# Kernel tuning notes

Measured on AMD Instinct MI355X. Metric: run time of the kernel, lower is better.

Reference implementation:

```python
import jax, jax.numpy as jnp
import numpy as np

N, C, H, W = 16, 256, 64, 64
KC, VC, HEADS = 256, 256, 8

def setup_inputs() -> dict:
    key = jax.random.key(0)
    ks = jax.random.split(key, 9)
    s = 0.02
    return {
        "x": jax.random.normal(ks[0], (N, C, H, W), dtype=jnp.float32),
        "Wk": jax.random.normal(ks[1], (KC, C), dtype=jnp.float32) * s,
        "bk": jax.random.normal(ks[2], (KC,), dtype=jnp.float32) * s,
        "Wq": jax.random.normal(ks[3], (KC, C), dtype=jnp.float32) * s,
        "bq": jax.random.normal(ks[4], (KC,), dtype=jnp.float32) * s,
        "Wv": jax.random.normal(ks[5], (VC, C), dtype=jnp.float32) * s,
        "bv": jax.random.normal(ks[6], (VC,), dtype=jnp.float32) * s,
        "Wr": jax.random.normal(ks[7], (C, VC), dtype=jnp.float32) * s,
        "br": jax.random.normal(ks[8], (C,), dtype=jnp.float32) * s,
    }

def reference(x, Wk, bk, Wq, bq, Wv, bv, Wr, br):
    n, c, h, w = x.shape
    hw = h * w
    hk = KC // HEADS   # per-head key channels
    hv = VC // HEADS   # per-head value channels
    # 1x1 convs as channel matmuls
    keys = jnp.einsum('oi,nihw->nohw', Wk, x) + bk[None, :, None, None]
    queries = jnp.einsum('oi,nihw->nohw', Wq, x) + bq[None, :, None, None]
    values = jnp.einsum('oi,nihw->nohw', Wv, x) + bv[None, :, None, None]
    # split heads: (n, heads, ch_per_head, hw)
    k = keys.reshape(n, HEADS, hk, hw)
    q = queries.reshape(n, HEADS, hk, hw)
    v = values.reshape(n, HEADS, hv, hw)
    k = jax.nn.softmax(k, axis=3)   # softmax over spatial positions
    q = jax.nn.softmax(q, axis=2)   # softmax over key channels
    # context: (n, heads, hk, hv)
    ctx = jnp.einsum('nhkl,nhvl->nhkv', k, v)
    # attended: (n, heads, hv, hw)
    att = jnp.einsum('nhkv,nhkl->nhvl', ctx, q)
    agg = att.reshape(n, VC, h, w)
    out = jnp.einsum('ov,nvhw->nohw', Wr, agg) + br[None, :, None, None] + x
    return out
```

## Files before the change

kernel.cpp:

```cpp
#include <hip/hip_runtime.h>

#define NB   16
#define CD   256
#define HWD  4096

typedef __attribute__((ext_vector_type(8))) short short8;
typedef __attribute__((ext_vector_type(4))) float f32x4;

static __device__ __forceinline__ float b2f(unsigned short u) {
  union { unsigned int i; float f; } x; x.i = ((unsigned int)u) << 16; return x.f;
}
static __device__ __forceinline__ unsigned short f2b(float f) {
  union { float f; unsigned int i; } x; x.f = f;
  return (unsigned short)((x.i + 0x7fffu + ((x.i >> 16) & 1u)) >> 16);
}

static __device__ __forceinline__ void gload16(const void* g, const unsigned short* l) {
  __builtin_amdgcn_global_load_lds(
      (const __attribute__((address_space(1))) void*)g,
      (__attribute__((address_space(3))) void*)l, 16, 0, 0);
}

__global__ __launch_bounds__(256)
void prep_kernel(const float* __restrict__ Wk, const float* __restrict__ Wq,
                 const float* __restrict__ Wv, unsigned short* __restrict__ Wc)
{
  int e4 = blockIdx.x * 256 + threadIdx.x;
  int base = e4 * 4;
  int w = base >> 16, off = base & 65535;
  const float* W = (w == 0) ? Wk : (w == 1) ? Wq : Wv;
  f32x4 v = *(const f32x4*)(W + off);
  unsigned int lo = (unsigned int)f2b(v.x) | ((unsigned int)f2b(v.y) << 16);
  unsigned int hi = (unsigned int)f2b(v.z) | ((unsigned int)f2b(v.w) << 16);
  *(uint2*)(Wc + base) = make_uint2(lo, hi);
}

__global__ __launch_bounds__(256)
void xt_kernel(const float* __restrict__ x, unsigned short* __restrict__ xT)
{
  __shared__ __align__(16) unsigned short T[64 * 80];
  const int t = threadIdx.x;
  const int l0 = blockIdx.x * 64, c0 = blockIdx.y * 64, n = blockIdx.z;
  const float* xn = x + (size_t)n * CD * HWD;
#pragma unroll
  for (int i = 0; i < 4; ++i) {
    int idx = t + i * 256;
    int c = idx >> 4, l4 = (idx & 15) * 4;
    f32x4 v = *(const f32x4*)(xn + (size_t)(c0 + c) * HWD + l0 + l4);
    T[(l4 + 0) * 80 + c] = f2b(v.x);
    T[(l4 + 1) * 80 + c] = f2b(v.y);
    T[(l4 + 2) * 80 + c] = f2b(v.z);
    T[(l4 + 3) * 80 + c] = f2b(v.w);
  }
  __syncthreads();
  unsigned short* dst = xT + ((size_t)n * HWD + l0) * CD + c0;
#pragma unroll
  for (int i = 0; i < 2; ++i) {
    int e = t + i * 256;
    int lr = e >> 3, c8 = (e & 7) * 8;
    *(short8*)(dst + (size_t)lr * CD + c8) = *(const short8*)(T + lr * 80 + c8);
  }
}

__global__ __launch_bounds__(256, 4)
void kv_kernel(const unsigned short* __restrict__ Wc,
               const unsigned short* __restrict__ xT,
               const float* __restrict__ bk, const float* __restrict__ bv,
               unsigned short* __restrict__ keys,
               unsigned short* __restrict__ vals)
{
  __shared__ __align__(16) unsigned short smem[17408];

  const int t  = threadIdx.x;
  const int lt = blockIdx.x;
  const int mt = blockIdx.y;
  const int n  = blockIdx.z;
  const int l0 = lt * 128;
  const int wsel   = mt >> 1;
  const int ocbase = (mt & 1) * 128;
  const int mstart = wsel ? (512 + ocbase) : ocbase;

  const unsigned short* Ag  = Wc;
  const unsigned short* Btn = xT + (size_t)n * HWD * CD;

  const int w = t >> 6, lane = t & 63;
  const int wr = (w >> 1) * 64, wc = (w & 1) * 64;
  const int lhi = lane >> 4, llo = lane & 15;

  f32x4 acc[4][4] = {};

  auto stage = [&](int buf, int ks) {
    unsigned short* As = smem + buf * 8192;
    unsigned short* Bs = As + 4096;
    const int k0 = ks * 32;
#pragma unroll
    for (int i = 0; i < 2; ++i) {
      int s   = t + i * 256;
      int row = s >> 2;
      int src = (((s ^ row) & 3)) << 3;
      gload16(Ag  + (size_t)(mstart + row) * CD + k0 + src, As + s * 8);
      gload16(Btn + (size_t)(l0 + row) * CD + k0 + src, Bs + s * 8);
    }
  };

  auto compute = [&](int buf) {
    const unsigned short* As = smem + buf * 8192;
    const unsigned short* Bs = As + 4096;
    const int slot = (lhi ^ (llo & 3)) * 8;
    short8 a[4], b[4];
#pragma unroll
    for (int mi = 0; mi < 4; ++mi)
      a[mi] = *(const short8*)(As + (wr + mi * 16 + llo) * 32 + slot);
#pragma unroll
    for (int ni = 0; ni < 4; ++ni)
      b[ni] = *(const short8*)(Bs + (wc + ni * 16 + llo) * 32 + slot);
#pragma unroll
    for (int mi = 0; mi < 4; ++mi)
#pragma unroll
      for (int ni = 0; ni < 4; ++ni)
        acc[mi][ni] = __builtin_amdgcn_mfma_f32_16x16x32_bf16(a[mi], b[ni], acc[mi][ni], 0, 0, 0);
  };

  stage(0, 0);
  __syncthreads();
#pragma unroll
  for (int ks = 0; ks < 8; ++ks) {
    if (ks < 7) stage((ks + 1) & 1, ks + 1);
    compute(ks & 1);
    __syncthreads();
  }

  const float* bias = wsel ? bv : bk;
#pragma unroll
  for (int mi = 0; mi < 4; ++mi)
#pragma unroll
    for (int r = 0; r < 4; ++r) {
      float bb = bias[ocbase + wr + mi * 16 + lhi * 4 + r];
#pragma unroll
      for (int ni = 0; ni < 4; ++ni) acc[mi][ni][r] += bb;
    }

  unsigned short* Co = smem;
#pragma unroll
  for (int mi = 0; mi < 4; ++mi)
#pragma unroll
    for (int ni = 0; ni < 4; ++ni) {
      int col = wc + ni * 16 + llo;
#pragma unroll
      for (int r = 0; r < 4; ++r) {
        int row = wr + mi * 16 + lhi * 4 + r;
        Co[row * 136 + col] = f2b(acc[mi][ni][r]);
      }
    }
  __syncthreads();
  unsigned short* dst = (wsel ? vals : keys) + ((size_t)(n * CD + ocbase)) * HWD + l0;
#pragma unroll
  for (int i = 0; i < 8; ++i) {
    int e = t + i * 256;
    int row = e >> 4, c8 = (e & 15) * 8;
    *(short8*)(dst + (size_t)row * HWD + c8) = *(const short8*)(Co + row * 136 + c8);
  }
}

__global__ __launch_bounds__(256)
void rowstats_kernel(const unsigned short* __restrict__ keys,
                     float* __restrict__ stats)
{
  __shared__ float red[8];
  const int r = blockIdx.x;
  const int t = threadIdx.x;
  const unsigned short* rowp = keys + (size_t)r * HWD;
  float v[16];
  float m = -1e30f;
#pragma unroll
  for (int i = 0; i < 2; ++i) {
    const short8 u = *(const short8*)(rowp + t * 8 + i * 2048);
#pragma unroll
    for (int j = 0; j < 8; ++j) {
      v[i * 8 + j] = b2f((unsigned short)u[j]);
      m = fmaxf(m, v[i * 8 + j]);
    }
  }
#pragma unroll
  for (int off = 1; off < 64; off <<= 1) m = fmaxf(m, __shfl_xor(m, off));
  if ((t & 63) == 0) red[t >> 6] = m;
  __syncthreads();
  m = fmaxf(fmaxf(red[0], red[1]), fmaxf(red[2], red[3]));
  float s = 0.f;
#pragma unroll
  for (int i = 0; i < 16; ++i) s += __expf(v[i] - m);
#pragma unroll
  for (int off = 1; off < 64; off <<= 1) s += __shfl_xor(s, off);
  if ((t & 63) == 0) red[4 + (t >> 6)] = s;
  __syncthreads();
  if (t == 0) {
    s = red[4] + red[5] + red[6] + red[7];
    stats[r * 2]     = m;
    stats[r * 2 + 1] = 1.f / s;
  }
}

__global__ __launch_bounds__(256)
void ctx_kernel(const unsigned short* __restrict__ keys,
                const unsigned short* __restrict__ vals,
                const float* __restrict__ stats,
                float* __restrict__ ctxp)
{
  __shared__ float Cs[4][32][33];
  const int hf = blockIdx.x;
  const int nh = blockIdx.y;
  const int n = nh >> 3, h = nh & 7;
  const int t = threadIdx.x, w = t >> 6, lane = t & 63;
  const int lhi = lane >> 4, llo = lane & 15;
  const int lbase = hf * 2048 + w * 512;

  const unsigned short* kr = keys + (size_t)(n * CD + h * 32) * HWD;
  const unsigned short* vr = vals + (size_t)(n * CD + h * 32) * HWD;

  float mx[2], inv[2];
#pragma unroll
  for (int mi = 0; mi < 2; ++mi) {
    int kc = mi * 16 + llo;
    mx[mi]  = stats[(n * CD + h * 32 + kc) * 2];
    inv[mi] = stats[(n * CD + h * 32 + kc) * 2 + 1];
  }

  f32x4 acc[2][2] = {};
  for (int ks = 0; ks < 16; ++ks) {
    const int loff = lbase + ks * 32 + lhi * 8;
    short8 a[2], b[2];
#pragma unroll
    for (int mi = 0; mi < 2; ++mi) {
      const short8 u = *(const short8*)(kr + (size_t)(mi * 16 + llo) * HWD + loff);
      short8 af;
#pragma unroll
      for (int j = 0; j < 8; ++j)
        af[j] = (short)f2b(__expf(b2f((unsigned short)u[j]) - mx[mi]) * inv[mi]);
      a[mi] = af;
    }
#pragma unroll
    for (int ni = 0; ni < 2; ++ni)
      b[ni] = *(const short8*)(vr + (size_t)(ni * 16 + llo) * HWD + loff);
    acc[0][0] = __builtin_amdgcn_mfma_f32_16x16x32_bf16(a[0], b[0], acc[0][0], 0, 0, 0);
    acc[0][1] = __builtin_amdgcn_mfma_f32_16x16x32_bf16(a[0], b[1], acc[0][1], 0, 0, 0);
    acc[1][0] = __builtin_amdgcn_mfma_f32_16x16x32_bf16(a[1], b[0], acc[1][0], 0, 0, 0);
    acc[1][1] = __builtin_amdgcn_mfma_f32_16x16x32_bf16(a[1], b[1], acc[1][1], 0, 0, 0);
  }

#pragma unroll
  for (int mi = 0; mi < 2; ++mi)
#pragma unroll
    for (int ni = 0; ni < 2; ++ni)
#pragma unroll
      for (int r = 0; r < 4; ++r)
        Cs[w][mi * 16 + lhi * 4 + r][ni * 16 + llo] = acc[mi][ni][r];
  __syncthreads();
#pragma unroll
  for (int i = 0; i < 4; ++i) {
    int e = t + i * 256;
    int kc = e >> 5, vc = e & 31;
    float sum = Cs[0][kc][vc] + Cs[1][kc][vc] + Cs[2][kc][vc] + Cs[3][kc][vc];
    ctxp[((size_t)hf * 128 + nh) * 1024 + e] = sum;
  }
}

__global__ __launch_bounds__(256)
void proj_kernel(const float* __restrict__ ctxp, const float* __restrict__ Wr,
                 unsigned short* __restrict__ M)
{
  __shared__ float cs[32][33];
  const int nh = blockIdx.x;
  const int n = nh >> 3, h = nh & 7;
  const int t = threadIdx.x;
#pragma unroll
  for (int i = 0; i < 4; ++i) {
    int e = t + i * 256;
    cs[e >> 5][e & 31] = ctxp[(size_t)nh * 1024 + e] + ctxp[((size_t)128 + nh) * 1024 + e];
  }
  __syncthreads();
  float wreg[32];
  const float* wp = Wr + (size_t)t * 256 + h * 32;
#pragma unroll
  for (int i = 0; i < 8; ++i) {
    f32x4 v = *(const f32x4*)(wp + i * 4);
    wreg[i * 4] = v.x; wreg[i * 4 + 1] = v.y; wreg[i * 4 + 2] = v.z; wreg[i * 4 + 3] = v.w;
  }
  unsigned short o16[32];
#pragma unroll
  for (int kc = 0; kc < 32; ++kc) {
    float s = 0.f;
#pragma unroll
    for (int vv = 0; vv < 32; ++vv) s += wreg[vv] * cs[kc][vv];
    o16[kc] = f2b(s);
  }
  unsigned short* mp = M + (size_t)(n * CD + t) * 256 + h * 32;
#pragma unroll
  for (int i = 0; i < 8; ++i) {
    unsigned int lo = (unsigned int)o16[i * 4]     | ((unsigned int)o16[i * 4 + 1] << 16);
    unsigned int hi = (unsigned int)o16[i * 4 + 2] | ((unsigned int)o16[i * 4 + 3] << 16);
    *(uint2*)(mp + i * 4) = make_uint2(lo, hi);
  }
}

__global__ __launch_bounds__(512, 1)
void qout_kernel(const unsigned short* __restrict__ Wc,
                 const unsigned short* __restrict__ M,
                 const unsigned short* __restrict__ xT,
                 const float* __restrict__ bq, const float* __restrict__ br,
                 const float* __restrict__ x, float* __restrict__ out)
{
  __shared__ __align__(16) unsigned short smem[49152];
  unsigned short* Bx = smem;

  const int t  = threadIdx.x;
  const int lt = blockIdx.x;
  const int n  = blockIdx.y;
  const int l0 = lt * 128;

  const unsigned short* Ag1 = Wc + 256 * CD;
  const unsigned short* Ag2 = M + (size_t)n * CD * 256;
  const unsigned short* Btn = xT + (size_t)n * HWD * CD;

  const int wid = t >> 6, lane = t & 63;
  const int wr = (wid & 3) * 64;
  const int wcl = (wid >> 2) * 64;
  const int lhi = lane >> 4, llo = lane & 15;

#pragma unroll
  for (int i = 0; i < 8; ++i) {
    int s = t + i * 512; int R = s >> 5; int sl = s & 31;
    int srcsl = (sl & 24) | ((sl ^ R) & 7);
    gload16(Btn + (size_t)(l0 + R) * CD + srcsl * 8, Bx + s * 8);
  }

  auto stageA = [&](const unsigned short* Ag, int buf, int ks) {
    unsigned short* Ad = smem + 32768 + buf * 8192;
#pragma unroll
    for (int i = 0; i < 2; ++i) {
      int s = t + i * 512; int R = s >> 2; int sl = s & 3;
      int srcsl = (sl ^ R) & 3;
      gload16(Ag + (size_t)R * CD + ks * 32 + srcsl * 8, Ad + s * 8);
    }
  };

  f32x4 acc[4][4] = {};
  auto computeStep = [&](int buf, int ks) {
    const unsigned short* Ad = smem + 32768 + buf * 8192;
    short8 a[4], b[4];
#pragma unroll
    for (int mi = 0; mi < 4; ++mi) {
      int R = wr + mi * 16 + llo;
      a[mi] = *(const short8*)(Ad + R * 32 + ((lhi ^ (R & 3)) << 3));
    }
#pragma unroll
    for (int ni = 0; ni < 4; ++ni) {
      int l = wcl + ni * 16 + llo;
      int jg = ks * 4 + lhi;
      int pj = (jg & 24) | ((jg ^ (l & 7)) & 7);
      b[ni] = *(const short8*)(Bx + l * 256 + pj * 8);
    }
#pragma unroll
    for (int mi = 0; mi < 4; ++mi)
#pragma unroll
      for (int ni = 0; ni < 4; ++ni)
        acc[mi][ni] = __builtin_amdgcn_mfma_f32_16x16x32_bf16(a[mi], b[ni], acc[mi][ni], 0, 0, 0);
  };

  stageA(Ag1, 0, 0);
  __syncthreads();
#pragma unroll
  for (int ks = 0; ks < 8; ++ks) {
    if (ks < 7) stageA(Ag1, (ks + 1) & 1, ks + 1);
    computeStep(ks & 1, ks);
    __syncthreads();
  }

  stageA(Ag2, 0, 0);

#pragma unroll
  for (int mi = 0; mi < 4; ++mi)
#pragma unroll
    for (int r = 0; r < 4; ++r) {
      float bb = bq[wr + mi * 16 + lhi * 4 + r];
#pragma unroll
      for (int ni = 0; ni < 4; ++ni) acc[mi][ni][r] += bb;
    }
#pragma unroll
  for (int g = 0; g < 2; ++g) {
#pragma unroll
    for (int ni = 0; ni < 4; ++ni) {
      float m = -1e30f;
#pragma unroll
      for (int mi = 2 * g; mi < 2 * g + 2; ++mi)
#pragma unroll
        for (int r = 0; r < 4; ++r) m = fmaxf(m, acc[mi][ni][r]);
      m = fmaxf(m, __shfl_xor(m, 16));
      m = fmaxf(m, __shfl_xor(m, 32));
      float s = 0.f;
#pragma unroll
      for (int mi = 2 * g; mi < 2 * g + 2; ++mi)
#pragma unroll
        for (int r = 0; r < 4; ++r) {
          float e = __expf(acc[mi][ni][r] - m);
          acc[mi][ni][r] = e;
          s += e;
        }
      s += __shfl_xor(s, 16);
      s += __shfl_xor(s, 32);
      float inv = 1.f / s;
#pragma unroll
      for (int mi = 2 * g; mi < 2 * g + 2; ++mi)
#pragma unroll
        for (int r = 0; r < 4; ++r) acc[mi][ni][r] *= inv;
    }
  }

#pragma unroll
  for (int mi = 0; mi < 4; ++mi) {
    int cb = wr + mi * 16 + lhi * 4;
    int cslot = cb >> 3;
#pragma unroll
    for (int ni = 0; ni < 4; ++ni) {
      int l = wcl + ni * 16 + llo;
      int pj = (cslot & 24) | ((cslot ^ (l & 7)) & 7);
      unsigned int u0 = (unsigned int)f2b(acc[mi][ni][0]) | ((unsigned int)f2b(acc[mi][ni][1]) << 16);
      unsigned int u1 = (unsigned int)f2b(acc[mi][ni][2]) | ((unsigned int)f2b(acc[mi][ni][3]) << 16);
      *(uint2*)(Bx + l * 256 + pj * 8 + (cb & 7)) = make_uint2(u0, u1);
    }
  }
  __syncthreads();

#pragma unroll
  for (int mi = 0; mi < 4; ++mi)
#pragma unroll
    for (int ni = 0; ni < 4; ++ni)
      acc[mi][ni] = f32x4{0.f, 0.f, 0.f, 0.f};
#pragma unroll
  for (int ks = 0; ks < 8; ++ks) {
    if (ks < 7) stageA(Ag2, (ks + 1) & 1, ks + 1);
    computeStep(ks & 1, ks);
    __syncthreads();
  }

  const float* xn = x + (size_t)n * CD * HWD;
  float* on = out + (size_t)n * CD * HWD;
#pragma unroll
  for (int mi = 0; mi < 4; ++mi)
#pragma unroll
    for (int r = 0; r < 4; ++r) {
      int row = wr + mi * 16 + lhi * 4 + r;
      float bb = br[row];
#pragma unroll
      for (int ni = 0; ni < 4; ++ni) {
        int col = l0 + wcl + ni * 16 + llo;
        size_t off = (size_t)row * HWD + col;
        on[off] = acc[mi][ni][r] + bb + xn[off];
      }
    }
}

extern "C" void kernel_launch(void* const* d_in, const int* in_sizes, int n_in,
                              void* d_out, int out_size, void* d_ws, size_t ws_size,
                              hipStream_t stream) {
  const float* x  = (const float*)d_in[0];
  const float* Wk = (const float*)d_in[1];
  const float* bk = (const float*)d_in[2];
  const float* Wq = (const float*)d_in[3];
  const float* bq = (const float*)d_in[4];
  const float* Wv = (const float*)d_in[5];
  const float* bv = (const float*)d_in[6];
  const float* Wr = (const float*)d_in[7];
  const float* br = (const float*)d_in[8];
  float* out = (float*)d_out;

  char* ws = (char*)d_ws;
  unsigned short* keys = (unsigned short*)(ws);
  unsigned short* vals = (unsigned short*)(ws + 33554432);
  unsigned short* xT   = (unsigned short*)(ws + 67108864);
  float* stats         = (float*)(ws + 100663296);
  float* ctxp          = (float*)(ws + 100696064);
  unsigned short* M    = (unsigned short*)(ws + 101744640);
  unsigned short* Wc   = (unsigned short*)(ws + 103841792);

  hipLaunchKernelGGL(prep_kernel, dim3(192), dim3(256), 0, stream, Wk, Wq, Wv, Wc);
  hipLaunchKernelGGL(xt_kernel, dim3(64, 4, NB), dim3(256), 0, stream, x, xT);
  hipLaunchKernelGGL(kv_kernel, dim3(32, 4, NB), dim3(256), 0, stream,
                     Wc, xT, bk, bv, keys, vals);
  hipLaunchKernelGGL(rowstats_kernel, dim3(NB * CD), dim3(256), 0, stream, keys, stats);
  hipLaunchKernelGGL(ctx_kernel, dim3(2, 128), dim3(256), 0, stream,
                     keys, vals, stats, ctxp);
  hipLaunchKernelGGL(proj_kernel, dim3(128), dim3(256), 0, stream, ctxp, Wr, M);
  hipLaunchKernelGGL(qout_kernel, dim3(32, NB), dim3(512), 0, stream,
                     Wc, M, xT, bq, br, x, out);
}
```

Measured before the change: 134.2 us.

## Split fused q/out GEMM, keep weight operand in registers, place xT in output buffer

The weight (A) operand of the kv, q and output GEMMs is now loaded once into registers, so only the activation tile is staged through LDS. kv_kernel switches to 512-thread blocks that each cover all 256 output channels. The former fused qout_kernel is split into q_kernel, which computes the query softmax and writes a transposed bf16 buffer, and out_kernel, which multiplies M by that buffer and adds bias and residual. The transposed x scratch is moved into the output buffer. This trades extra global traffic for the q intermediate and higher register pressure against less LDS staging and better occupancy.

```diff
diff --git a/kernel.cpp b/kernel.cpp
--- a/kernel.cpp
+++ b/kernel.cpp
@@ -62,320 +62,150 @@
   }
 }
 
-__global__ __launch_bounds__(256, 4)
+__global__ __launch_bounds__(512, 2)
 void kv_kernel(const unsigned short* __restrict__ Wc,
                const unsigned short* __restrict__ xT,
                const float* __restrict__ bk, const float* __restrict__ bv,
                unsigned short* __restrict__ keys,
                unsigned short* __restrict__ vals)
 {
-  __shared__ __align__(16) unsigned short smem[17408];
-
-  const int t  = threadIdx.x;
-  const int lt = blockIdx.x;
-  const int mt = blockIdx.y;
-  const int n  = blockIdx.z;
-  const int l0 = lt * 128;
-  const int wsel   = mt >> 1;
-  const int ocbase = (mt & 1) * 128;
-  const int mstart = wsel ? (512 + ocbase) : ocbase;
+  __shared__ __align__(16) unsigned short smem[34816];
+
+  const int t   = threadIdx.x;
+  const int lt  = blockIdx.x;
+  const int sel = blockIdx.y;
+  const int n   = blockIdx.z;
+  const int l0  = lt * 128;
+  const int abase = sel * 512;
 
   const unsigned short* Ag  = Wc;
   const unsigned short* Btn = xT + (size_t)n * HWD * CD;
 
-  const int w = t >> 6, lane = t & 63;
-  const int wr = (w >> 1) * 64, wc = (w & 1) * 64;
+  const int wid = t >> 6, lane = t & 63;
+  const int wr = (wid >> 1) * 64;
+  const int wcl = (wid & 1) * 64;
   const int lhi = lane >> 4, llo = lane & 15;
 
+  short8 a[4][8];
+#pragma unroll
+  for (int mi = 0; mi < 4; ++mi)
+#pragma unroll
+    for (int ks = 0; ks < 8; ++ks) {
+      int R = abase + wr + mi * 16 + llo;
+      a[mi][ks] = *(const short8*)(Ag + (size_t)R * CD + ks * 32 + lhi * 8);
+    }
+
+  auto stageB = [&](int buf, int ks) {
+    unsigned short* Bs = smem + buf * 4096;
+    int s = t;
+    int row = s >> 2;
+    int src = ((s & 3) ^ (row & 3)) << 3;
+    gload16(Btn + (size_t)(l0 + row) * CD + ks * 32 + src, Bs + s * 8);
+  };
+
   f32x4 acc[4][4] = {};
-
-  auto stage = [&](int buf, int ks) {
-    unsigned short* As = smem + buf * 8192;
-    unsigned short* Bs = As + 4096;
-    const int k0 = ks * 32;
-#pragma unroll
-    for (int i = 0; i < 2; ++i) {
-      int s   = t + i * 256;
-      int row = s >> 2;
-      int src = (((s ^ row) & 3)) << 3;
-      gload16(Ag  + (size_t)(mstart + row) * CD + k0 + src, As + s * 8);
-      gload16(Btn + (size_t)(l0 + row) * CD + k0 + src, Bs + s * 8);
-    }
-  };
-
-  auto compute = [&](int buf) {
-    const unsigned short* As = smem + buf * 8192;
-    const unsigned short* Bs = As + 4096;
-    const int slot = (lhi ^ (llo & 3)) * 8;
-    short8 a[4], b[4];
+  stageB(0, 0);
+  __syncthreads();
+#pragma unroll
+  for (int ks = 0; ks < 8; ++ks) {
+    if (ks < 7) stageB((ks + 1) & 1, ks + 1);
+    const unsigned short* Bs = smem + (ks & 1) * 4096;
+    short8 b[4];
+#pragma unroll
+    for (int ni = 0; ni < 4; ++ni) {
+      int l = wcl + ni * 16 + llo;
+      b[ni] = *(const short8*)(Bs + l * 32 + ((lhi ^ (l & 3)) << 3));
+    }
 #pragma unroll
     for (int mi = 0; mi < 4; ++mi)
-      a[mi] = *(const short8*)(As + (wr + mi * 16 + llo) * 32 + slot);
-#pragma unroll
-    for (int ni = 0; ni < 4; ++ni)
-      b[ni] = *(const short8*)(Bs + (wc + ni * 16 + llo) * 32 + slot);
-#pragma unroll
-    for (int mi = 0; mi < 4; ++mi)
 #pragma unroll
       for (int ni = 0; ni < 4; ++ni)
-        acc[mi][ni] = __builtin_amdgcn_mfma_f32_16x16x32_bf16(a[mi], b[ni], acc[mi][ni], 0, 0, 0);
-  };
-
-  stage(0, 0);
-  __syncthreads();
-#pragma unroll
-  for (int ks = 0; ks < 8; ++ks) {
-    if (ks < 7) stage((ks + 1) & 1, ks + 1);
-    compute(ks & 1);
+        acc[mi][ni] = __builtin_amdgcn_mfma_f32_16x16x32_bf16(a[mi][ks], b[ni], acc[mi][ni], 0, 0, 0);
     __syncthreads();
   }
 
-  const float* bias = wsel ? bv : bk;
+  const float* bias = sel ? bv : bk;
+  unsigned short* Co = smem;
 #pragma unroll
   for (int mi = 0; mi < 4; ++mi)
 #pragma unroll
     for (int r = 0; r < 4; ++r) {
-      float bb = bias[ocbase + wr + mi * 16 + lhi * 4 + r];
-#pragma unroll
-      for (int ni = 0; ni < 4; ++ni) acc[mi][ni][r] += bb;
-    }
-
-  unsigned short* Co = smem;
-#pragma unroll
-  for (int mi = 0; mi < 4; ++mi)
-#pragma unroll
-    for (int ni = 0; ni < 4; ++ni) {
-      int col = wc + ni * 16 + llo;
-#pragma unroll
-      for (int r = 0; r < 4; ++r) {
-        int row = wr + mi * 16 + lhi * 4 + r;
-        Co[row * 136 + col] = f2b(acc[mi][ni][r]);
+      int row = wr + mi * 16 + lhi * 4 + r;
+      float bb = bias[row];
+#pragma unroll
+      for (int ni = 0; ni < 4; ++ni) {
+        int col = wcl + ni * 16 + llo;
+        Co[row * 136 + col] = f2b(acc[mi][ni][r] + bb);
       }
     }
   __syncthreads();
-  unsigned short* dst = (wsel ? vals : keys) + ((size_t)(n * CD + ocbase)) * HWD + l0;
+  unsigned short* dst = (sel ? vals : keys) + (size_t)n * CD * HWD + l0;
 #pragma unroll
   for (int i = 0; i < 8; ++i) {
-    int e = t + i * 256;
+    int e = t + i * 512;
     int row = e >> 4, c8 = (e & 15) * 8;
     *(short8*)(dst + (size_t)row * HWD + c8) = *(const short8*)(Co + row * 136 + c8);
   }
 }
 
-__global__ __launch_bounds__(256)
-void rowstats_kernel(const unsigned short* __restrict__ keys,
-                     float* __restrict__ stats)
-{
-  __shared__ float red[8];
-  const int r = blockIdx.x;
-  const int t = threadIdx.x;
-  const unsigned short* rowp = keys + (size_t)r * HWD;
-  float v[16];
-  float m = -1e30f;
-#pragma unroll
-  for (int i = 0; i < 2; ++i) {
-    const short8 u = *(const short8*)(rowp + t * 8 + i * 2048);
-#pragma unroll
-    for (int j = 0; j < 8; ++j) {
-      v[i * 8 + j] = b2f((unsigned short)u[j]);
-      m = fmaxf(m, v[i * 8 + j]);
-    }
-  }
-#pragma unroll
-  for (int off = 1; off < 64; off <<= 1) m = fmaxf(m, __shfl_xor(m, off));
-  if ((t & 63) == 0) red[t >> 6] = m;
-  __syncthreads();
-  m = fmaxf(fmaxf(red[0], red[1]), fmaxf(red[2], red[3]));
-  float s = 0.f;
-#pragma unroll
-  for (int i = 0; i < 16; ++i) s += __expf(v[i] - m);
-#pragma unroll
-  for (int off = 1; off < 64; off <<= 1) s += __shfl_xor(s, off);
-  if ((t & 63) == 0) red[4 + (t >> 6)] = s;
-  __syncthreads();
-  if (t == 0) {
-    s = red[4] + red[5] + red[6] + red[7];
-    stats[r * 2]     = m;
-    stats[r * 2 + 1] = 1.f / s;
-  }
-}
-
-__global__ __launch_bounds__(256)
-void ctx_kernel(const unsigned short* __restrict__ keys,
-                const unsigned short* __restrict__ vals,
-                const float* __restrict__ stats,
-                float* __restrict__ ctxp)
-{
-  __shared__ float Cs[4][32][33];
-  const int hf = blockIdx.x;
-  const int nh = blockIdx.y;
-  const int n = nh >> 3, h = nh & 7;
-  const int t = threadIdx.x, w = t >> 6, lane = t & 63;
-  const int lhi = lane >> 4, llo = lane & 15;
-  const int lbase = hf * 2048 + w * 512;
-
-  const unsigned short* kr = keys + (size_t)(n * CD + h * 32) * HWD;
-  const unsigned short* vr = vals + (size_t)(n * CD + h * 32) * HWD;
-
-  float mx[2], inv[2];
-#pragma unroll
-  for (int mi = 0; mi < 2; ++mi) {
-    int kc = mi * 16 + llo;
-    mx[mi]  = stats[(n * CD + h * 32 + kc) * 2];
-    inv[mi] = stats[(n * CD + h * 32 + kc) * 2 + 1];
-  }
-
-  f32x4 acc[2][2] = {};
-  for (int ks = 0; ks < 16; ++ks) {
-    const int loff = lbase + ks * 32 + lhi * 8;
-    short8 a[2], b[2];
-#pragma unroll
-    for (int mi = 0; mi < 2; ++mi) {
-      const short8 u = *(const short8*)(kr + (size_t)(mi * 16 + llo) * HWD + loff);
-      short8 af;
-#pragma unroll
-      for (int j = 0; j < 8; ++j)
-        af[j] = (short)f2b(__expf(b2f((unsigned short)u[j]) - mx[mi]) * inv[mi]);
-      a[mi] = af;
-    }
-#pragma unroll
-    for (int ni = 0; ni < 2; ++ni)
-      b[ni] = *(const short8*)(vr + (size_t)(ni * 16 + llo) * HWD + loff);
-    acc[0][0] = __builtin_amdgcn_mfma_f32_16x16x32_bf16(a[0], b[0], acc[0][0], 0, 0, 0);
-    acc[0][1] = __builtin_amdgcn_mfma_f32_16x16x32_bf16(a[0], b[1], acc[0][1], 0, 0, 0);
-    acc[1][0] = __builtin_amdgcn_mfma_f32_16x16x32_bf16(a[1], b[0], acc[1][0], 0, 0, 0);
-    acc[1][1] = __builtin_amdgcn_mfma_f32_16x16x32_bf16(a[1], b[1], acc[1][1], 0, 0, 0);
-  }
-
-#pragma unroll
-  for (int mi = 0; mi < 2; ++mi)
-#pragma unroll
-    for (int ni = 0; ni < 2; ++ni)
-#pragma unroll
-      for (int r = 0; r < 4; ++r)
-        Cs[w][mi * 16 + lhi * 4 + r][ni * 16 + llo] = acc[mi][ni][r];
-  __syncthreads();
-#pragma unroll
-  for (int i = 0; i < 4; ++i) {
-    int e = t + i * 256;
-    int kc = e >> 5, vc = e & 31;
-    float sum = Cs[0][kc][vc] + Cs[1][kc][vc] + Cs[2][kc][vc] + Cs[3][kc][vc];
-    ctxp[((size_t)hf * 128 + nh) * 1024 + e] = sum;
-  }
-}
-
-__global__ __launch_bounds__(256)
-void proj_kernel(const float* __restrict__ ctxp, const float* __restrict__ Wr,
-                 unsigned short* __restrict__ M)
-{
-  __shared__ float cs[32][33];
-  const int nh = blockIdx.x;
-  const int n = nh >> 3, h = nh & 7;
-  const int t = threadIdx.x;
-#pragma unroll
-  for (int i = 0; i < 4; ++i) {
-    int e = t + i * 256;
-    cs[e >> 5][e & 31] = ctxp[(size_t)nh * 1024 + e] + ctxp[((size_t)128 + nh) * 1024 + e];
-  }
-  __syncthreads();
-  float wreg[32];
-  const float* wp = Wr + (size_t)t * 256 + h * 32;
-#pragma unroll
-  for (int i = 0; i < 8; ++i) {
-    f32x4 v = *(const f32x4*)(wp + i * 4);
-    wreg[i * 4] = v.x; wreg[i * 4 + 1] = v.y; wreg[i * 4 + 2] = v.z; wreg[i * 4 + 3] = v.w;
-  }
-  unsigned short o16[32];
-#pragma unroll
-  for (int kc = 0; kc < 32; ++kc) {
-    float s = 0.f;
-#pragma unroll
-    for (int vv = 0; vv < 32; ++vv) s += wreg[vv] * cs[kc][vv];
-    o16[kc] = f2b(s);
-  }
-  unsigned short* mp = M + (size_t)(n * CD + t) * 256 + h * 32;
-#pragma unroll
-  for (int i = 0; i < 8; ++i) {
-    unsigned int lo = (unsigned int)o16[i * 4]     | ((unsigned int)o16[i * 4 + 1] << 16);
-    unsigned int hi = (unsigned int)o16[i * 4 + 2] | ((unsigned int)o16[i * 4 + 3] << 16);
-    *(uint2*)(mp + i * 4) = make_uint2(lo, hi);
-  }
-}
-
-__global__ __launch_bounds__(512, 1)
-void qout_kernel(const unsigned short* __restrict__ Wc,
-                 const unsigned short* __restrict__ M,
-                 const unsigned short* __restrict__ xT,
-                 const float* __restrict__ bq, const float* __restrict__ br,
-                 const float* __restrict__ x, float* __restrict__ out)
-{
-  __shared__ __align__(16) unsigned short smem[49152];
-  unsigned short* Bx = smem;
+__global__ __launch_bounds__(512, 2)
+void q_kernel(const unsigned short* __restrict__ Wc,
+              const unsigned short* __restrict__ xT,
+              const float* __restrict__ bq,
+              unsigned short* __restrict__ qsmT)
+{
+  __shared__ __align__(16) unsigned short smem[33792];
 
   const int t  = threadIdx.x;
   const int lt = blockIdx.x;
   const int n  = blockIdx.y;
   const int l0 = lt * 128;
 
-  const unsigned short* Ag1 = Wc + 256 * CD;
-  const unsigned short* Ag2 = M + (size_t)n * CD * 256;
+  const unsigned short* Ag  = Wc + 256 * CD;
   const unsigned short* Btn = xT + (size_t)n * HWD * CD;
 
   const int wid = t >> 6, lane = t & 63;
-  const int wr = (wid & 3) * 64;
-  const int wcl = (wid >> 2) * 64;
+  const int wr = (wid >> 1) * 64;
+  const int wcl = (wid & 1) * 64;
   const int lhi = lane >> 4, llo = lane & 15;
 
-#pragma unroll
-  for (int i = 0; i < 8; ++i) {
-    int s = t + i * 512; int R = s >> 5; int sl = s & 31;
-    int srcsl = (sl & 24) | ((sl ^ R) & 7);
-    gload16(Btn + (size_t)(l0 + R) * CD + srcsl * 8, Bx + s * 8);
-  }
-
-  auto stageA = [&](const unsigned short* Ag, int buf, int ks) {
-    unsigned short* Ad = smem + 32768 + buf * 8192;
-#pragma unroll
-    for (int i = 0; i < 2; ++i) {
-      int s = t + i * 512; int R = s >> 2; int sl = s & 3;
-      int srcsl = (sl ^ R) & 3;
-      gload16(Ag + (size_t)R * CD + ks * 32 + srcsl * 8, Ad + s * 8);
-    }
+  short8 a[4][8];
+#pragma unroll
+  for (int mi = 0; mi < 4; ++mi)
+#pragma unroll
+    for (int ks = 0; ks < 8; ++ks) {
+      int R = wr + mi * 16 + llo;
+      a[mi][ks] = *(const short8*)(Ag + (size_t)R * CD + ks * 32 + lhi * 8);
+    }
+
+  auto stageB = [&](int buf, int ks) {
+    unsigned short* Bs = smem + buf * 4096;
+    int s = t;
+    int row = s >> 2;
+    int src = ((s & 3) ^ (row & 3)) << 3;
+    gload16(Btn + (size_t)(l0 + row) * CD + ks * 32 + src, Bs + s * 8);
   };
 
   f32x4 acc[4][4] = {};
-  auto computeStep = [&](int buf, int ks) {
-    const unsigned short* Ad = smem + 32768 + buf * 8192;
-    short8 a[4], b[4];
-#pragma unroll
-    for (int mi = 0; mi < 4; ++mi) {
-      int R = wr + mi * 16 + llo;
-      a[mi] = *(const short8*)(Ad + R * 32 + ((lhi ^ (R & 3)) << 3));
-    }
+  stageB(0, 0);
+  __syncthreads();
+#pragma unroll
+  for (int ks = 0; ks < 8; ++ks) {
+    if (ks < 7) stageB((ks + 1) & 1, ks + 1);
+    const unsigned short* Bs = smem + (ks & 1) * 4096;
+    short8 b[4];
 #pragma unroll
     for (int ni = 0; ni < 4; ++ni) {
       int l = wcl + ni * 16 + llo;
-      int jg = ks * 4 + lhi;
-      int pj = (jg & 24) | ((jg ^ (l & 7)) & 7);
-      b[ni] = *(const short8*)(Bx + l * 256 + pj * 8);
+      b[ni] = *(const short8*)(Bs + l * 32 + ((lhi ^ (l & 3)) << 3));
     }
 #pragma unroll
     for (int mi = 0; mi < 4; ++mi)
 #pragma unroll
       for (int ni = 0; ni < 4; ++ni)
-        acc[mi][ni] = __builtin_amdgcn_mfma_f32_16x16x32_bf16(a[mi], b[ni], acc[mi][ni], 0, 0, 0);
-  };
-
-  stageA(Ag1, 0, 0);
-  __syncthreads();
-#pragma unroll
-  for (int ks = 0; ks < 8; ++ks) {
-    if (ks < 7) stageA(Ag1, (ks + 1) & 1, ks + 1);
-    computeStep(ks & 1, ks);
+        acc[mi][ni] = __builtin_amdgcn_mfma_f32_16x16x32_bf16(a[mi][ks], b[ni], acc[mi][ni], 0, 0, 0);
     __syncthreads();
   }
-
-  stageA(Ag2, 0, 0);
 
 #pragma unroll
   for (int mi = 0; mi < 4; ++mi)
@@ -385,6 +215,7 @@
 #pragma unroll
       for (int ni = 0; ni < 4; ++ni) acc[mi][ni][r] += bb;
     }
+
 #pragma unroll
   for (int g = 0; g < 2; ++g) {
 #pragma unroll
@@ -415,30 +246,225 @@
     }
   }
 
-#pragma unroll
-  for (int mi = 0; mi < 4; ++mi) {
-    int cb = wr + mi * 16 + lhi * 4;
-    int cslot = cb >> 3;
+  unsigned short* Co2 = smem;
+#pragma unroll
+  for (int mi = 0; mi < 4; ++mi)
 #pragma unroll
     for (int ni = 0; ni < 4; ++ni) {
       int l = wcl + ni * 16 + llo;
-      int pj = (cslot & 24) | ((cslot ^ (l & 7)) & 7);
-      unsigned int u0 = (unsigned int)f2b(acc[mi][ni][0]) | ((unsigned int)f2b(acc[mi][ni][1]) << 16);
-      unsigned int u1 = (unsigned int)f2b(acc[mi][ni][2]) | ((unsigned int)f2b(acc[mi][ni][3]) << 16);
-      *(uint2*)(Bx + l * 256 + pj * 8 + (cb & 7)) = make_uint2(u0, u1);
-    }
-  }
-  __syncthreads();
-
-#pragma unroll
-  for (int mi = 0; mi < 4; ++mi)
-#pragma unroll
-    for (int ni = 0; ni < 4; ++ni)
-      acc[mi][ni] = f32x4{0.f, 0.f, 0.f, 0.f};
+#pragma unroll
+      for (int r = 0; r < 4; ++r) {
+        int row = wr + mi * 16 + lhi * 4 + r;
+        Co2[l * 264 + row] = f2b(acc[mi][ni][r]);
+      }
+    }
+  __syncthreads();
+  unsigned short* dst = qsmT + ((size_t)n * HWD + l0) * CD;
+#pragma unroll
+  for (int i = 0; i < 8; ++i) {
+    int e = t + i * 512;
+    int l = e >> 5, c8 = (e & 31) * 8;
+    *(short8*)(dst + (size_t)l * CD + c8) = *(const short8*)(Co2 + l * 264 + c8);
+  }
+}
+
+__global__ __launch_bounds__(256)
+void rowstats_kernel(const unsigned short* __restrict__ keys,
+                     float* __restrict__ stats)
+{
+  __shared__ float red[8];
+  const int r = blockIdx.x;
+  const int t = threadIdx.x;
+  const unsigned short* rowp = keys + (size_t)r * HWD;
+  float v[16];
+  float m = -1e30f;
+#pragma unroll
+  for (int i = 0; i < 2; ++i) {
+    const short8 u = *(const short8*)(rowp + t * 8 + i * 2048);
+#pragma unroll
+    for (int j = 0; j < 8; ++j) {
+      v[i * 8 + j] = b2f((unsigned short)u[j]);
+      m = fmaxf(m, v[i * 8 + j]);
+    }
+  }
+#pragma unroll
+  for (int off = 1; off < 64; off <<= 1) m = fmaxf(m, __shfl_xor(m, off));
+  if ((t & 63) == 0) red[t >> 6] = m;
+  __syncthreads();
+  m = fmaxf(fmaxf(red[0], red[1]), fmaxf(red[2], red[3]));
+  float s = 0.f;
+#pragma unroll
+  for (int i = 0; i < 16; ++i) s += __expf(v[i] - m);
+#pragma unroll
+  for (int off = 1; off < 64; off <<= 1) s += __shfl_xor(s, off);
+  if ((t & 63) == 0) red[4 + (t >> 6)] = s;
+  __syncthreads();
+  if (t == 0) {
+    s = red[4] + red[5] + red[6] + red[7];
+    stats[r * 2]     = m;
+    stats[r * 2 + 1] = 1.f / s;
+  }
+}
+
+__global__ __launch_bounds__(256)
+void ctx_kernel(const unsigned short* __restrict__ keys,
+                const unsigned short* __restrict__ vals,
+                const float* __restrict__ stats,
+                float* __restrict__ ctxp)
+{
+  __shared__ float Cs[4][32][33];
+  const int hf = blockIdx.x;
+  const int nh = blockIdx.y;
+  const int n = nh >> 3, h = nh & 7;
+  const int t = threadIdx.x, w = t >> 6, lane = t & 63;
+  const int lhi = lane >> 4, llo = lane & 15;
+  const int lbase = hf * 2048 + w * 512;
+
+  const unsigned short* kr = keys + (size_t)(n * CD + h * 32) * HWD;
+  const unsigned short* vr = vals + (size_t)(n * CD + h * 32) * HWD;
+
+  float mx[2], inv[2];
+#pragma unroll
+  for (int mi = 0; mi < 2; ++mi) {
+    int kc = mi * 16 + llo;
+    mx[mi]  = stats[(n * CD + h * 32 + kc) * 2];
+    inv[mi] = stats[(n * CD + h * 32 + kc) * 2 + 1];
+  }
+
+  f32x4 acc[2][2] = {};
+  for (int ks = 0; ks < 16; ++ks) {
+    const int loff = lbase + ks * 32 + lhi * 8;
+    short8 a[2], b[2];
+#pragma unroll
+    for (int mi = 0; mi < 2; ++mi) {
+      const short8 u = *(const short8*)(kr + (size_t)(mi * 16 + llo) * HWD + loff);
+      short8 af;
+#pragma unroll
+      for (int j = 0; j < 8; ++j)
+        af[j] = (short)f2b(__expf(b2f((unsigned short)u[j]) - mx[mi]) * inv[mi]);
+      a[mi] = af;
+    }
+#pragma unroll
+    for (int ni = 0; ni < 2; ++ni)
+      b[ni] = *(const short8*)(vr + (size_t)(ni * 16 + llo) * HWD + loff);
+    acc[0][0] = __builtin_amdgcn_mfma_f32_16x16x32_bf16(a[0], b[0], acc[0][0], 0, 0, 0);
+    acc[0][1] = __builtin_amdgcn_mfma_f32_16x16x32_bf16(a[0], b[1], acc[0][1], 0, 0, 0);
+    acc[1][0] = __builtin_amdgcn_mfma_f32_16x16x32_bf16(a[1], b[0], acc[1][0], 0, 0, 0);
+    acc[1][1] = __builtin_amdgcn_mfma_f32_16x16x32_bf16(a[1], b[1], acc[1][1], 0, 0, 0);
+  }
+
+#pragma unroll
+  for (int mi = 0; mi < 2; ++mi)
+#pragma unroll
+    for (int ni = 0; ni < 2; ++ni)
+#pragma unroll
+      for (int r = 0; r < 4; ++r)
+        Cs[w][mi * 16 + lhi * 4 + r][ni * 16 + llo] = acc[mi][ni][r];
+  __syncthreads();
+#pragma unroll
+  for (int i = 0; i < 4; ++i) {
+    int e = t + i * 256;
+    int kc = e >> 5, vc = e & 31;
+    float sum = Cs[0][kc][vc] + Cs[1][kc][vc] + Cs[2][kc][vc] + Cs[3][kc][vc];
+    ctxp[((size_t)hf * 128 + nh) * 1024 + e] = sum;
+  }
+}
+
+__global__ __launch_bounds__(256)
+void proj_kernel(const float* __restrict__ ctxp, const float* __restrict__ Wr,
+                 unsigned short* __restrict__ M)
+{
+  __shared__ float cs[32][33];
+  const int nh = blockIdx.x;
+  const int n = nh >> 3, h = nh & 7;
+  const int t = threadIdx.x;
+#pragma unroll
+  for (int i = 0; i < 4; ++i) {
+    int e = t + i * 256;
+    cs[e >> 5][e & 31] = ctxp[(size_t)nh * 1024 + e] + ctxp[((size_t)128 + nh) * 1024 + e];
+  }
+  __syncthreads();
+  float wreg[32];
+  const float* wp = Wr + (size_t)t * 256 + h * 32;
+#pragma unroll
+  for (int i = 0; i < 8; ++i) {
+    f32x4 v = *(const f32x4*)(wp + i * 4);
+    wreg[i * 4] = v.x; wreg[i * 4 + 1] = v.y; wreg[i * 4 + 2] = v.z; wreg[i * 4 + 3] = v.w;
+  }
+  unsigned short o16[32];
+#pragma unroll
+  for (int kc = 0; kc < 32; ++kc) {
+    float s = 0.f;
+#pragma unroll
+    for (int vv = 0; vv < 32; ++vv) s += wreg[vv] * cs[kc][vv];
+    o16[kc] = f2b(s);
+  }
+  unsigned short* mp = M + (size_t)(n * CD + t) * 256 + h * 32;
+#pragma unroll
+  for (int i = 0; i < 8; ++i) {
+    unsigned int lo = (unsigned int)o16[i * 4]     | ((unsigned int)o16[i * 4 + 1] << 16);
+    unsigned int hi = (unsigned int)o16[i * 4 + 2] | ((unsigned int)o16[i * 4 + 3] << 16);
+    *(uint2*)(mp + i * 4) = make_uint2(lo, hi);
+  }
+}
+
+__global__ __launch_bounds__(512, 2)
+void out_kernel(const unsigned short* __restrict__ M,
+                const unsigned short* __restrict__ qsmT,
+                const float* __restrict__ br,
+                const float* __restrict__ x,
+                float* __restrict__ out)
+{
+  __shared__ __align__(16) unsigned short smem[8192];
+
+  const int t  = threadIdx.x;
+  const int lt = blockIdx.x;
+  const int n  = blockIdx.y;
+  const int l0 = lt * 128;
+
+  const unsigned short* Ag  = M + (size_t)n * CD * 256;
+  const unsigned short* Btn = qsmT + (size_t)n * HWD * CD;
+
+  const int wid = t >> 6, lane = t & 63;
+  const int wr = (wid >> 1) * 64;
+  const int wcl = (wid & 1) * 64;
+  const int lhi = lane >> 4, llo = lane & 15;
+
+  short8 a[4][8];
+#pragma unroll
+  for (int mi = 0; mi < 4; ++mi)
+#pragma unroll
+    for (int ks = 0; ks < 8; ++ks) {
+      int R = wr + mi * 16 + llo;
+      a[mi][ks] = *(const short8*)(Ag + (size_t)R * CD + ks * 32 + lhi * 8);
+    }
+
+  auto stageB = [&](int buf, int ks) {
+    unsigned short* Bs = smem + buf * 4096;
+    int s = t;
+    int row = s >> 2;
+    int src = ((s & 3) ^ (row & 3)) << 3;
+    gload16(Btn + (size_t)(l0 + row) * CD + ks * 32 + src, Bs + s * 8);
+  };
+
+  f32x4 acc[4][4] = {};
+  stageB(0, 0);
+  __syncthreads();
 #pragma unroll
   for (int ks = 0; ks < 8; ++ks) {
-    if (ks < 7) stageA(Ag2, (ks + 1) & 1, ks + 1);
-    computeStep(ks & 1, ks);
+    if (ks < 7) stageB((ks + 1) & 1, ks + 1);
+    const unsigned short* Bs = smem + (ks & 1) * 4096;
+    short8 b[4];
+#pragma unroll
+    for (int ni = 0; ni < 4; ++ni) {
+      int l = wcl + ni * 16 + llo;
+      b[ni] = *(const short8*)(Bs + l * 32 + ((lhi ^ (l & 3)) << 3));
+    }
+#pragma unroll
+    for (int mi = 0; mi < 4; ++mi)
+#pragma unroll
+      for (int ni = 0; ni < 4; ++ni)
+        acc[mi][ni] = __builtin_amdgcn_mfma_f32_16x16x32_bf16(a[mi][ks], b[ni], acc[mi][ni], 0, 0, 0);
     __syncthreads();
   }
 
@@ -476,20 +502,23 @@
   char* ws = (char*)d_ws;
   unsigned short* keys = (unsigned short*)(ws);
   unsigned short* vals = (unsigned short*)(ws + 33554432);
-  unsigned short* xT   = (unsigned short*)(ws + 67108864);
+  unsigned short* qsmT = (unsigned short*)(ws + 67108864);
   float* stats         = (float*)(ws + 100663296);
   float* ctxp          = (float*)(ws + 100696064);
   unsigned short* M    = (unsigned short*)(ws + 101744640);
   unsigned short* Wc   = (unsigned short*)(ws + 103841792);
+  unsigned short* xT   = (unsigned short*)d_out;
 
   hipLaunchKernelGGL(prep_kernel, dim3(192), dim3(256), 0, stream, Wk, Wq, Wv, Wc);
   hipLaunchKernelGGL(xt_kernel, dim3(64, 4, NB), dim3(256), 0, stream, x, xT);
-  hipLaunchKernelGGL(kv_kernel, dim3(32, 4, NB), dim3(256), 0, stream,
+  hipLaunchKernelGGL(kv_kernel, dim3(32, 2, NB), dim3(512), 0, stream,
                      Wc, xT, bk, bv, keys, vals);
+  hipLaunchKernelGGL(q_kernel, dim3(32, NB), dim3(512), 0, stream,
+                     Wc, xT, bq, qsmT);
   hipLaunchKernelGGL(rowstats_kernel, dim3(NB * CD), dim3(256), 0, stream, keys, stats);
   hipLaunchKernelGGL(ctx_kernel, dim3(2, 128), dim3(256), 0, stream,
                      keys, vals, stats, ctxp);
   hipLaunchKernelGGL(proj_kernel, dim3(128), dim3(256), 0, stream, ctxp, Wr, M);
-  hipLaunchKernelGGL(qout_kernel, dim3(32, NB), dim3(512), 0, stream,
-                     Wc, M, xT, bq, br, x, out);
-}
+  hipLaunchKernelGGL(out_kernel, dim3(32, NB), dim3(512), 0, stream,
+                     M, qsmT, br, x, out);
+}
```

Result: slower. 187.4 us (+39.7%).
